# Kernel optimization log

Measured on AMD Instinct MI355X. Metric: run time of the kernel, lower is better.

## Reference

```python
import jax, jax.numpy as jnp
import numpy as np

D_MODEL = 384
HEAD_SIZE = 64
CONTEXT = 100


def setup_inputs() -> dict:
    key = jax.random.key(0)
    kx, kq, kk, kv = jax.random.split(key, 4)
    x = jax.random.normal(kx, (1024, CONTEXT, D_MODEL), dtype=jnp.float32)
    s = 1.0 / np.sqrt(D_MODEL)
    Wq = jax.random.normal(kq, (D_MODEL, HEAD_SIZE), dtype=jnp.float32) * s
    Wk = jax.random.normal(kk, (D_MODEL, HEAD_SIZE), dtype=jnp.float32) * s
    Wv = jax.random.normal(kv, (D_MODEL, HEAD_SIZE), dtype=jnp.float32) * s
    return {"x": x, "Wq": Wq, "Wk": Wk, "Wv": Wv}


def reference(x, Wq, Wk, Wv):
    B, T, C = x.shape
    q = jnp.einsum('btc,ch->bth', x, Wq)
    k = jnp.einsum('btc,ch->bth', x, Wk)
    v = jnp.einsum('btc,ch->bth', x, Wv)
    # Faithful to source bug: divide by d**(-0.5) == multiply by sqrt(d)
    scale = jnp.asarray(k.shape[-1], x.dtype) ** 0.5
    wei = jnp.einsum('bth,bsh->bts', q, k) * scale  # [B,T,T]
    causal = jnp.tril(jnp.ones((T, T), dtype=bool))
    wei = jnp.where(causal, wei, -jnp.inf)
    wei = jax.nn.softmax(wei, axis=-1)
    # dropout: eval mode (identity)
    return jnp.einsum('bts,bsh->bth', wei, v)
```

## Files before the change

kernel.cpp:

```cpp
#include <hip/hip_runtime.h>
#include <hip/hip_fp16.h>

#define T_CTX 100
#define C_DIM 384
#define H_DIM 64

typedef _Float16 half8   __attribute__((ext_vector_type(8)));
typedef _Float16 half4_t __attribute__((ext_vector_type(4)));
typedef float    f32x4   __attribute__((ext_vector_type(4)));

#define QH_OFF 0
#define QL_OFF 8192
#define KH_OFF 16384
#define KL_OFF 23552
#define VT_OFF 30720
#define XS_OFF 0
#define PS_OFF 0
#define SMEM_BYTES 77824

__global__ void prep_w_kernel(const float* __restrict__ Wq,
                              const float* __restrict__ Wk,
                              const float* __restrict__ Wv,
                              _Float16* __restrict__ wf_hi,
                              _Float16* __restrict__ wf_lo) {
    int idx = blockIdx.x * 256 + threadIdx.x;
    if (idx >= 9216) return;
    int lane  = idx & 63;
    int chunk = (idx >> 6) % 12;
    int jt    = idx / (64 * 12);
    int col   = jt * 16 + (lane & 15);
    const float* W = (col < 64) ? Wq : ((col < 128) ? Wk : Wv);
    int h = col & 63;
    int cbase = chunk * 32 + (lane >> 4) * 8;
    #pragma unroll
    for (int e = 0; e < 8; ++e) {
        float f = W[(size_t)(cbase + e) * H_DIM + h];
        _Float16 hi = (_Float16)f;
        _Float16 lo = (_Float16)(f - (float)hi);
        size_t o = (size_t)idx * 8 + e;
        wf_hi[o] = hi;
        wf_lo[o] = lo;
    }
}

__global__ __launch_bounds__(512, 4)
void head_kernel(const float* __restrict__ x,
                 const _Float16* __restrict__ wf_hi,
                 const _Float16* __restrict__ wf_lo,
                 float* __restrict__ out) {
    extern __shared__ _Float16 sm[];

    const int b    = blockIdx.x;
    const int tid  = threadIdx.x;
    const int lane = tid & 63;
    const int wid  = tid >> 6;
    const int l15  = lane & 15;
    const int lg   = lane >> 4;
    const int mh   = wid >> 2;
    const int nw   = wid & 3;

    const float* xb = x + (size_t)b * T_CTX * C_DIM;
    _Float16* xs = sm + XS_OFF;

    f32x4 acc[4][3];
    #pragma unroll
    for (int i = 0; i < 4; ++i)
        #pragma unroll
        for (int j = 0; j < 3; ++j)
            acc[i][j] = (f32x4){0.f, 0.f, 0.f, 0.f};

    #pragma unroll
    for (int s = 0; s < 2; ++s) {
        int f4  = tid + s * 512;
        int row = f4 >> 3;
        int c4  = f4 & 7;
        f32x4 v = (f32x4){0.f, 0.f, 0.f, 0.f};
        if (row < T_CTX) v = *(const f32x4*)(xb + row * C_DIM + c4 * 4);
        half4_t hh, ll;
        #pragma unroll
        for (int u = 0; u < 4; ++u) {
            _Float16 h = (_Float16)v[u];
            hh[u] = h;
            ll[u] = (_Float16)(v[u] - (float)h);
        }
        int o = row * 40 + c4 * 4;
        *(half4_t*)(xs + o)        = hh;
        *(half4_t*)(xs + 5120 + o) = ll;
    }
    __syncthreads();

    for (int kc = 0; kc < 12; ++kc) {
        const int nk = kc + 1;
        f32x4 ld[2];
        if (nk < 12) {
            #pragma unroll
            for (int s = 0; s < 2; ++s) {
                int f4  = tid + s * 512;
                int row = f4 >> 3;
                int c4  = f4 & 7;
                ld[s] = (f32x4){0.f, 0.f, 0.f, 0.f};
                if (row < T_CTX) ld[s] = *(const f32x4*)(xb + row * C_DIM + nk * 32 + c4 * 4);
            }
        }
        const _Float16* xh = xs + (kc & 1) * 10240;
        const _Float16* xl = xh + 5120;
        half8 ah[4], al[4];
        #pragma unroll
        for (int i = 0; i < 4; ++i) {
            int o = (mh * 64 + i * 16 + l15) * 40 + lg * 8;
            ah[i] = *(const half8*)(xh + o);
            al[i] = *(const half8*)(xl + o);
        }
        #pragma unroll
        for (int jj = 0; jj < 3; ++jj) {
            size_t o = ((size_t)((nw * 3 + jj) * 12 + kc) * 64 + lane) * 8;
            half8 bh = *(const half8*)(wf_hi + o);
            half8 bl = *(const half8*)(wf_lo + o);
            #pragma unroll
            for (int i = 0; i < 4; ++i) {
                acc[i][jj] = __builtin_amdgcn_mfma_f32_16x16x32_f16(ah[i], bh, acc[i][jj], 0, 0, 0);
                acc[i][jj] = __builtin_amdgcn_mfma_f32_16x16x32_f16(al[i], bh, acc[i][jj], 0, 0, 0);
                acc[i][jj] = __builtin_amdgcn_mfma_f32_16x16x32_f16(ah[i], bl, acc[i][jj], 0, 0, 0);
            }
        }
        if (nk < 12) {
            #pragma unroll
            for (int s = 0; s < 2; ++s) {
                int f4  = tid + s * 512;
                int row = f4 >> 3;
                int c4  = f4 & 7;
                half4_t hh, ll;
                #pragma unroll
                for (int u = 0; u < 4; ++u) {
                    _Float16 h = (_Float16)ld[s][u];
                    hh[u] = h;
                    ll[u] = (_Float16)(ld[s][u] - (float)h);
                }
                int o = row * 40 + c4 * 4;
                *(half4_t*)(xs + (nk & 1) * 10240 + o)        = hh;
                *(half4_t*)(xs + (nk & 1) * 10240 + 5120 + o) = ll;
            }
        }
        __syncthreads();
    }

    #pragma unroll
    for (int i = 0; i < 4; ++i) {
        #pragma unroll
        for (int jj = 0; jj < 3; ++jj) {
            int ncol = nw * 48 + jj * 16 + l15;
            #pragma unroll
            for (int r = 0; r < 4; ++r) {
                int row = mh * 64 + i * 16 + lg * 4 + r;
                float val = acc[i][jj][r];
                if (ncol < 64) {
                    int off = (row >> 4) * 1024 + (ncol >> 5) * 512
                            + (((ncol >> 3) & 3) * 16 + (row & 15)) * 8 + (ncol & 7);
                    _Float16 h = (_Float16)val;
                    sm[QH_OFF + off] = h;
                    sm[QL_OFF + off] = (_Float16)(val - (float)h);
                } else if (ncol < 128) {
                    if (row < 112) {
                        int hc = ncol - 64;
                        int off = (row >> 4) * 1024 + (hc >> 5) * 512
                                + (((hc >> 3) & 3) * 16 + (row & 15)) * 8 + (hc & 7);
                        _Float16 h = (_Float16)val;
                        sm[KH_OFF + off] = h;
                        sm[KL_OFF + off] = (_Float16)(val - (float)h);
                    }
                } else {
                    int hc = ncol - 128;
                    int off = (hc >> 4) * 2048 + (row >> 5) * 512
                            + (((row >> 3) & 3) * 16 + (hc & 15)) * 8 + (row & 7);
                    sm[VT_OFF + off] = (_Float16)val;
                }
            }
        }
    }
    __syncthreads();

    f32x4 sacc[7];
    #pragma unroll
    for (int j = 0; j < 7; ++j) sacc[j] = (f32x4){0.f, 0.f, 0.f, 0.f};

    #pragma unroll
    for (int kk = 0; kk < 2; ++kk) {
        half8 qh = *(const half8*)(sm + QH_OFF + wid * 1024 + kk * 512 + lane * 8);
        half8 ql = *(const half8*)(sm + QL_OFF + wid * 1024 + kk * 512 + lane * 8);
        #pragma unroll
        for (int j = 0; j < 7; ++j) {
            half8 kh = *(const half8*)(sm + KH_OFF + j * 1024 + kk * 512 + lane * 8);
            half8 kl = *(const half8*)(sm + KL_OFF + j * 1024 + kk * 512 + lane * 8);
            sacc[j] = __builtin_amdgcn_mfma_f32_16x16x32_f16(qh, kh, sacc[j], 0, 0, 0);
            sacc[j] = __builtin_amdgcn_mfma_f32_16x16x32_f16(ql, kh, sacc[j], 0, 0, 0);
            sacc[j] = __builtin_amdgcn_mfma_f32_16x16x32_f16(qh, kl, sacc[j], 0, 0, 0);
        }
    }

    float rmax[4] = {-1e30f, -1e30f, -1e30f, -1e30f};
    float sv[7][4];
    #pragma unroll
    for (int j = 0; j < 7; ++j) {
        int key = j * 16 + l15;
        #pragma unroll
        for (int r = 0; r < 4; ++r) {
            int row = wid * 16 + lg * 4 + r;
            float s = (key <= row && key < T_CTX) ? sacc[j][r] * 8.0f : -1e30f;
            sv[j][r] = s;
            rmax[r] = fmaxf(rmax[r], s);
        }
    }
    #pragma unroll
    for (int r = 0; r < 4; ++r) {
        #pragma unroll
        for (int d = 1; d < 16; d <<= 1)
            rmax[r] = fmaxf(rmax[r], __shfl_xor(rmax[r], d, 64));
    }

    __syncthreads();

    float rsum[4] = {0.f, 0.f, 0.f, 0.f};
    #pragma unroll
    for (int j = 0; j < 7; ++j) {
        int key = j * 16 + l15;
        #pragma unroll
        for (int r = 0; r < 4; ++r) {
            float p = __expf(sv[j][r] - rmax[r]);
            rsum[r] += p;
            int a = lg * 4 + r;
            int off = wid * 2048 + (key >> 5) * 512
                    + (((key >> 3) & 3) * 16 + a) * 8 + (key & 7);
            sm[PS_OFF + off] = (_Float16)p;
        }
    }
    #pragma unroll
    for (int r = 0; r < 4; ++r) {
        int key = 112 + l15;
        int a = lg * 4 + r;
        int off = wid * 2048 + (key >> 5) * 512
                + (((key >> 3) & 3) * 16 + a) * 8 + (key & 7);
        sm[PS_OFF + off] = (_Float16)0.f;
        #pragma unroll
        for (int d = 1; d < 16; d <<= 1)
            rsum[r] += __shfl_xor(rsum[r], d, 64);
    }
    __syncthreads();

    f32x4 oacc[4];
    #pragma unroll
    for (int j = 0; j < 4; ++j) oacc[j] = (f32x4){0.f, 0.f, 0.f, 0.f};
    #pragma unroll
    for (int kk = 0; kk < 4; ++kk) {
        half8 pa = *(const half8*)(sm + PS_OFF + wid * 2048 + kk * 512 + lane * 8);
        #pragma unroll
        for (int jh = 0; jh < 4; ++jh) {
            half8 vb = *(const half8*)(sm + VT_OFF + jh * 2048 + kk * 512 + lane * 8);
            oacc[jh] = __builtin_amdgcn_mfma_f32_16x16x32_f16(pa, vb, oacc[jh], 0, 0, 0);
        }
    }
    #pragma unroll
    for (int jh = 0; jh < 4; ++jh) {
        #pragma unroll
        for (int r = 0; r < 4; ++r) {
            int t = wid * 16 + lg * 4 + r;
            if (t < T_CTX)
                out[((size_t)b * T_CTX + t) * H_DIM + jh * 16 + l15] = oacc[jh][r] / rsum[r];
        }
    }
}

extern "C" void kernel_launch(void* const* d_in, const int* in_sizes, int n_in,
                              void* d_out, int out_size, void* d_ws, size_t ws_size,
                              hipStream_t stream) {
    const float* x  = (const float*)d_in[0];
    const float* Wq = (const float*)d_in[1];
    const float* Wk = (const float*)d_in[2];
    const float* Wv = (const float*)d_in[3];

    _Float16* wf_hi = (_Float16*)d_ws;
    _Float16* wf_lo = wf_hi + (size_t)9216 * 8;

    prep_w_kernel<<<36, 256, 0, stream>>>(Wq, Wk, Wv, wf_hi, wf_lo);

    (void)hipFuncSetAttribute((const void*)head_kernel,
                              hipFuncAttributeMaxDynamicSharedMemorySize, SMEM_BYTES);
    head_kernel<<<1024, 512, SMEM_BYTES, stream>>>(x, wf_hi, wf_lo, (float*)d_out);
}
```

Measured before the change: 77.39 us.

## Load x fragments directly from global into registers, drop LDS staging and V low-part MFMAs

The QKV projection no longer stages x through double-buffered shared memory with a barrier per K-chunk. Each wave now loads its own x rows from global memory and splits them into hi/lo fp16 fragments in registers. Waves for the second row half skip the fully padded fourth tile, and the V projection uses only the hi×hi product instead of three-term compensation. Padded V rows are zeroed explicitly and the final division becomes a reciprocal multiply. The cost is redundant global loads of x across the four column waves and lower precision for V.

```diff
diff --git a/kernel.cpp b/kernel.cpp
--- a/kernel.cpp
+++ b/kernel.cpp
@@ -6,7 +6,7 @@
 #define H_DIM 64
 
 typedef _Float16 half8   __attribute__((ext_vector_type(8)));
-typedef _Float16 half4_t __attribute__((ext_vector_type(4)));
+typedef _Float16 half2_t __attribute__((ext_vector_type(2)));
 typedef float    f32x4   __attribute__((ext_vector_type(4)));
 
 #define QH_OFF 0
@@ -14,7 +14,6 @@
 #define KH_OFF 16384
 #define KL_OFF 23552
 #define VT_OFF 30720
-#define XS_OFF 0
 #define PS_OFF 0
 #define SMEM_BYTES 77824
 
@@ -43,6 +42,16 @@
     }
 }
 
+__device__ inline void cvt_hilo(f32x4 a, f32x4 c, half8& hh, half8& ll) {
+    float f[8] = {a[0], a[1], a[2], a[3], c[0], c[1], c[2], c[3]};
+    #pragma unroll
+    for (int u = 0; u < 8; ++u) {
+        _Float16 h = (_Float16)f[u];
+        hh[u] = h;
+        ll[u] = (_Float16)(f[u] - (float)h);
+    }
+}
+
 __global__ __launch_bounds__(512, 4)
 void head_kernel(const float* __restrict__ x,
                  const _Float16* __restrict__ wf_hi,
@@ -59,107 +68,85 @@
     const int mh   = wid >> 2;
     const int nw   = wid & 3;
 
+    const int tl0 = nw * 2;
+    const int tl1 = nw * 2 + 1;
+    const int tlv = 8 + nw;
+    const int NI  = (mh == 0) ? 4 : 3;
+
     const float* xb = x + (size_t)b * T_CTX * C_DIM;
-    _Float16* xs = sm + XS_OFF;
-
-    f32x4 acc[4][3];
-    #pragma unroll
-    for (int i = 0; i < 4; ++i)
-        #pragma unroll
-        for (int j = 0; j < 3; ++j)
-            acc[i][j] = (f32x4){0.f, 0.f, 0.f, 0.f};
-
-    #pragma unroll
-    for (int s = 0; s < 2; ++s) {
-        int f4  = tid + s * 512;
-        int row = f4 >> 3;
-        int c4  = f4 & 7;
-        f32x4 v = (f32x4){0.f, 0.f, 0.f, 0.f};
-        if (row < T_CTX) v = *(const f32x4*)(xb + row * C_DIM + c4 * 4);
-        half4_t hh, ll;
-        #pragma unroll
-        for (int u = 0; u < 4; ++u) {
-            _Float16 h = (_Float16)v[u];
-            hh[u] = h;
-            ll[u] = (_Float16)(v[u] - (float)h);
-        }
-        int o = row * 40 + c4 * 4;
-        *(half4_t*)(xs + o)        = hh;
-        *(half4_t*)(xs + 5120 + o) = ll;
-    }
-    __syncthreads();
-
+
+    f32x4 acc0[4], acc1[4], accv[4];
+    #pragma unroll
+    for (int i = 0; i < 4; ++i) {
+        acc0[i] = (f32x4){0.f,0.f,0.f,0.f};
+        acc1[i] = (f32x4){0.f,0.f,0.f,0.f};
+        accv[i] = (f32x4){0.f,0.f,0.f,0.f};
+    }
+
+    #pragma unroll 1
     for (int kc = 0; kc < 12; ++kc) {
-        const int nk = kc + 1;
-        f32x4 ld[2];
-        if (nk < 12) {
-            #pragma unroll
-            for (int s = 0; s < 2; ++s) {
-                int f4  = tid + s * 512;
-                int row = f4 >> 3;
-                int c4  = f4 & 7;
-                ld[s] = (f32x4){0.f, 0.f, 0.f, 0.f};
-                if (row < T_CTX) ld[s] = *(const f32x4*)(xb + row * C_DIM + nk * 32 + c4 * 4);
+        const size_t wo0 = ((size_t)(tl0 * 12 + kc) * 64 + lane) * 8;
+        const size_t wo1 = ((size_t)(tl1 * 12 + kc) * 64 + lane) * 8;
+        const size_t wov = ((size_t)(tlv * 12 + kc) * 64 + lane) * 8;
+        half8 b0h = *(const half8*)(wf_hi + wo0);
+        half8 b0l = *(const half8*)(wf_lo + wo0);
+        half8 b1h = *(const half8*)(wf_hi + wo1);
+        half8 b1l = *(const half8*)(wf_lo + wo1);
+        half8 bvh = *(const half8*)(wf_hi + wov);
+
+        half8 ah[4], al[4];
+        #pragma unroll
+        for (int i = 0; i < 4; ++i) {
+            if (i >= NI) break;
+            int row = mh * 64 + i * 16 + l15;
+            f32x4 xa = (f32x4){0.f,0.f,0.f,0.f};
+            f32x4 xc = (f32x4){0.f,0.f,0.f,0.f};
+            if (row < T_CTX) {
+                const float* p = xb + (size_t)row * C_DIM + kc * 32 + lg * 8;
+                xa = *(const f32x4*)p;
+                xc = *(const f32x4*)(p + 4);
             }
-        }
-        const _Float16* xh = xs + (kc & 1) * 10240;
-        const _Float16* xl = xh + 5120;
-        half8 ah[4], al[4];
+            cvt_hilo(xa, xc, ah[i], al[i]);
+        }
+
         #pragma unroll
         for (int i = 0; i < 4; ++i) {
-            int o = (mh * 64 + i * 16 + l15) * 40 + lg * 8;
-            ah[i] = *(const half8*)(xh + o);
-            al[i] = *(const half8*)(xl + o);
-        }
-        #pragma unroll
-        for (int jj = 0; jj < 3; ++jj) {
-            size_t o = ((size_t)((nw * 3 + jj) * 12 + kc) * 64 + lane) * 8;
-            half8 bh = *(const half8*)(wf_hi + o);
-            half8 bl = *(const half8*)(wf_lo + o);
-            #pragma unroll
-            for (int i = 0; i < 4; ++i) {
-                acc[i][jj] = __builtin_amdgcn_mfma_f32_16x16x32_f16(ah[i], bh, acc[i][jj], 0, 0, 0);
-                acc[i][jj] = __builtin_amdgcn_mfma_f32_16x16x32_f16(al[i], bh, acc[i][jj], 0, 0, 0);
-                acc[i][jj] = __builtin_amdgcn_mfma_f32_16x16x32_f16(ah[i], bl, acc[i][jj], 0, 0, 0);
-            }
-        }
-        if (nk < 12) {
-            #pragma unroll
-            for (int s = 0; s < 2; ++s) {
-                int f4  = tid + s * 512;
-                int row = f4 >> 3;
-                int c4  = f4 & 7;
-                half4_t hh, ll;
-                #pragma unroll
-                for (int u = 0; u < 4; ++u) {
-                    _Float16 h = (_Float16)ld[s][u];
-                    hh[u] = h;
-                    ll[u] = (_Float16)(ld[s][u] - (float)h);
-                }
-                int o = row * 40 + c4 * 4;
-                *(half4_t*)(xs + (nk & 1) * 10240 + o)        = hh;
-                *(half4_t*)(xs + (nk & 1) * 10240 + 5120 + o) = ll;
-            }
-        }
-        __syncthreads();
-    }
-
-    #pragma unroll
-    for (int i = 0; i < 4; ++i) {
-        #pragma unroll
-        for (int jj = 0; jj < 3; ++jj) {
-            int ncol = nw * 48 + jj * 16 + l15;
+            if (i >= NI) break;
+            acc0[i] = __builtin_amdgcn_mfma_f32_16x16x32_f16(ah[i], b0h, acc0[i], 0, 0, 0);
+            acc0[i] = __builtin_amdgcn_mfma_f32_16x16x32_f16(al[i], b0h, acc0[i], 0, 0, 0);
+            acc0[i] = __builtin_amdgcn_mfma_f32_16x16x32_f16(ah[i], b0l, acc0[i], 0, 0, 0);
+            acc1[i] = __builtin_amdgcn_mfma_f32_16x16x32_f16(ah[i], b1h, acc1[i], 0, 0, 0);
+            acc1[i] = __builtin_amdgcn_mfma_f32_16x16x32_f16(al[i], b1h, acc1[i], 0, 0, 0);
+            acc1[i] = __builtin_amdgcn_mfma_f32_16x16x32_f16(ah[i], b1l, acc1[i], 0, 0, 0);
+            accv[i] = __builtin_amdgcn_mfma_f32_16x16x32_f16(ah[i], bvh, accv[i], 0, 0, 0);
+        }
+    }
+
+    {
+        int jh = tid >> 7;
+        int w2 = (tid & 127) * 2;
+        *(half2_t*)(sm + VT_OFF + jh * 2048 + 1792 + w2) = (half2_t){(_Float16)0.f, (_Float16)0.f};
+    }
+
+    #pragma unroll
+    for (int tsel = 0; tsel < 3; ++tsel) {
+        const int tl = (tsel == 0) ? tl0 : (tsel == 1) ? tl1 : tlv;
+        f32x4* at = (tsel == 0) ? acc0 : (tsel == 1) ? acc1 : accv;
+        const int ncol = tl * 16 + l15;
+        #pragma unroll
+        for (int i = 0; i < 4; ++i) {
+            if (i >= NI) break;
             #pragma unroll
             for (int r = 0; r < 4; ++r) {
                 int row = mh * 64 + i * 16 + lg * 4 + r;
-                float val = acc[i][jj][r];
-                if (ncol < 64) {
+                float val = at[i][r];
+                if (tl < 4) {
                     int off = (row >> 4) * 1024 + (ncol >> 5) * 512
                             + (((ncol >> 3) & 3) * 16 + (row & 15)) * 8 + (ncol & 7);
                     _Float16 h = (_Float16)val;
                     sm[QH_OFF + off] = h;
                     sm[QL_OFF + off] = (_Float16)(val - (float)h);
-                } else if (ncol < 128) {
+                } else if (tl < 8) {
                     if (row < 112) {
                         int hc = ncol - 64;
                         int off = (row >> 4) * 1024 + (hc >> 5) * 512
@@ -181,7 +168,7 @@
 
     f32x4 sacc[7];
     #pragma unroll
-    for (int j = 0; j < 7; ++j) sacc[j] = (f32x4){0.f, 0.f, 0.f, 0.f};
+    for (int j = 0; j < 7; ++j) sacc[j] = (f32x4){0.f,0.f,0.f,0.f};
 
     #pragma unroll
     for (int kk = 0; kk < 2; ++kk) {
@@ -248,7 +235,7 @@
 
     f32x4 oacc[4];
     #pragma unroll
-    for (int j = 0; j < 4; ++j) oacc[j] = (f32x4){0.f, 0.f, 0.f, 0.f};
+    for (int j = 0; j < 4; ++j) oacc[j] = (f32x4){0.f,0.f,0.f,0.f};
     #pragma unroll
     for (int kk = 0; kk < 4; ++kk) {
         half8 pa = *(const half8*)(sm + PS_OFF + wid * 2048 + kk * 512 + lane * 8);
@@ -258,13 +245,16 @@
             oacc[jh] = __builtin_amdgcn_mfma_f32_16x16x32_f16(pa, vb, oacc[jh], 0, 0, 0);
         }
     }
+    float rinv[4];
+    #pragma unroll
+    for (int r = 0; r < 4; ++r) rinv[r] = 1.0f / rsum[r];
     #pragma unroll
     for (int jh = 0; jh < 4; ++jh) {
         #pragma unroll
         for (int r = 0; r < 4; ++r) {
             int t = wid * 16 + lg * 4 + r;
             if (t < T_CTX)
-                out[((size_t)b * T_CTX + t) * H_DIM + jh * 16 + l15] = oacc[jh][r] / rsum[r];
+                out[((size_t)b * T_CTX + t) * H_DIM + jh * 16 + l15] = oacc[jh][r] * rinv[r];
         }
     }
 }
```

Measured after the change: 104.7 us. +35.3%, slower.
